# Performance work log

Measured on AMD Instinct MI355X. Metric: run time of the kernel, lower is better.

Reference implementation:

```python
import jax, jax.numpy as jnp
import numpy as np
import math

EMBED_DIM = 1024
NUM_HEADS = 16
HEAD_DIM = EMBED_DIM // NUM_HEADS
TGT_LEN = 1024
BSZ = 4


def setup_inputs() -> dict:
    key = jax.random.key(0)
    ks = jax.random.split(key, 7)
    # xavier_uniform for in_proj_weight [3E, E]
    limit = math.sqrt(6.0 / (3 * EMBED_DIM + EMBED_DIM))
    in_proj_weight = jax.random.uniform(ks[0], (3 * EMBED_DIM, EMBED_DIM), jnp.float32, -limit, limit)
    in_proj_bias = jnp.zeros((3 * EMBED_DIM,), jnp.float32)
    # out_proj: torch Linear default init (kaiming-uniform-ish); bias zeroed by _reset_parameters
    lim_o = 1.0 / math.sqrt(EMBED_DIM)
    out_proj_weight = jax.random.uniform(ks[1], (EMBED_DIM, EMBED_DIM), jnp.float32, -lim_o, lim_o)
    out_proj_bias = jnp.zeros((EMBED_DIM,), jnp.float32)
    query = jax.random.normal(ks[2], (TGT_LEN, BSZ, EMBED_DIM), jnp.float32)
    key_t = jax.random.normal(ks[3], (TGT_LEN, BSZ, EMBED_DIM), jnp.float32)
    value = jax.random.normal(ks[4], (TGT_LEN, BSZ, EMBED_DIM), jnp.float32)
    return {"query": query, "key": key_t, "value": value,
            "in_proj_weight": in_proj_weight, "in_proj_bias": in_proj_bias,
            "out_proj_weight": out_proj_weight, "out_proj_bias": out_proj_bias}


def reference(query, key, value, in_proj_weight, in_proj_bias, out_proj_weight, out_proj_bias):
    tgt_len, bsz, embed_dim = query.shape
    src_len = key.shape[0]
    w_q, w_k, w_v = jnp.split(in_proj_weight, 3, axis=0)
    b_q, b_k, b_v = jnp.split(in_proj_bias, 3, axis=0)
    q = query @ w_q.T + b_q  # [T, B, E]
    k = key @ w_k.T + b_k    # [S, B, E]
    v = value @ w_v.T + b_v  # [S, B, E]
    # [T, B*H, D] -> [B*H, T, D]
    q = q.reshape(tgt_len, bsz * NUM_HEADS, HEAD_DIM).transpose(1, 0, 2)
    k = k.reshape(src_len, bsz * NUM_HEADS, HEAD_DIM).transpose(1, 0, 2)
    v = v.reshape(src_len, bsz * NUM_HEADS, HEAD_DIM).transpose(1, 0, 2)
    q = q / math.sqrt(embed_dim)  # NOTE: scales by sqrt(embed_dim), not head_dim (faithful)
    attn = jax.nn.sigmoid(jnp.einsum('btd,bsd->bts', q, k))  # [B*H, T, S]
    attn_output = jnp.einsum('bts,bsd->btd', attn, v)         # [B*H, T, D]
    attn_output = attn_output.transpose(1, 0, 2).reshape(tgt_len, bsz, embed_dim)
    attn_output = attn_output @ out_proj_weight.T + out_proj_bias
    return attn_output, attn
```

## Files before the change

### kernel.cpp

```cpp
#include <hip/hip_runtime.h>
#include <stdint.h>

typedef unsigned short u16;
typedef __bf16 bf16x8 __attribute__((ext_vector_type(8)));
typedef float f32x4 __attribute__((ext_vector_type(4)));

__device__ __forceinline__ u16 f2bf(float f) {
  union { float f; uint32_t u; } v; v.f = f;
  uint32_t u = v.u;
  return (u16)((u + 0x7FFFu + ((u >> 16) & 1u)) >> 16);
}

__device__ __forceinline__ float fast_sigmoid(float x) {
  float e = __builtin_amdgcn_exp2f(x * -1.4426950408889634f);
  return __builtin_amdgcn_rcpf(1.0f + e);
}

__device__ __forceinline__ void cp16(const void* g, void* lds) {
  __builtin_amdgcn_global_load_lds(
      (const __attribute__((address_space(1))) uint32_t*)(uintptr_t)g,
      (__attribute__((address_space(3))) uint32_t*)(uint32_t)(uintptr_t)lds,
      16, 0, 0);
}

__global__ __launch_bounds__(256) void cvt_all(
    const float* __restrict__ q, const float* __restrict__ k,
    const float* __restrict__ v, const float* __restrict__ iw,
    const float* __restrict__ ow, u16* __restrict__ xq,
    u16* __restrict__ win, u16* __restrict__ wout) {
  int i = blockIdx.x * 256 + threadIdx.x;
  const float* s;
  u16* d;
  int off;
  if (i < 2097152) {
    if (i < 1048576) { s = q; d = xq; off = i; }
    else { s = k; d = xq + 4194304; off = i - 1048576; }
  } else if (i < 3145728) { s = v; d = xq + 8388608; off = i - 2097152; }
  else if (i < 3932160) { s = iw; d = win; off = i - 3145728; }
  else { s = ow; d = wout; off = i - 3932160; }
  float4 f = ((const float4*)s)[off];
  uint2 p;
  p.x = (uint32_t)f2bf(f.x) | ((uint32_t)f2bf(f.y) << 16);
  p.y = (uint32_t)f2bf(f.z) | ((uint32_t)f2bf(f.w) << 16);
  ((uint2*)d)[off] = p;
}

__device__ __forceinline__ void gemm128(const u16* __restrict__ A,
                                        const u16* __restrict__ Bt,
                                        int m0, int n0, int K,
                                        u16* As, u16* Bs, f32x4 acc[4][4]) {
  const int tid = threadIdx.x;
  const int l = tid & 63, w = tid >> 6;
  const int wr = w >> 1, wc = w & 1;
  const int quad = l >> 4, c = l & 15;
  const f32x4 zero = {0.f, 0.f, 0.f, 0.f};
  for (int i = 0; i < 4; ++i)
    for (int j = 0; j < 4; ++j) acc[i][j] = zero;

  for (int k0 = 0; k0 < K; k0 += 64) {
    __syncthreads();
#pragma unroll
    for (int p = 0; p < 4; ++p) {
      int q = p * 256 + tid;
      int row = q >> 3;
      int jj = (q & 7) ^ (row & 7);
      int ldsbase = (p * 256 + (tid & ~63)) * 8;
      cp16(A + (size_t)(m0 + row) * K + k0 + jj * 8, As + ldsbase);
      cp16(Bt + (size_t)(n0 + row) * K + k0 + jj * 8, Bs + ldsbase);
    }
    __syncthreads();
#pragma unroll
    for (int kk = 0; kk < 2; ++kk) {
      bf16x8 af[4], bf[4];
#pragma unroll
      for (int mt = 0; mt < 4; ++mt) {
        int row = wr * 64 + mt * 16 + c;
        af[mt] = *(const bf16x8*)(As + row * 64 + ((((kk << 2) + quad)) ^ (c & 7)) * 8);
      }
#pragma unroll
      for (int nt = 0; nt < 4; ++nt) {
        int row = wc * 64 + nt * 16 + c;
        bf[nt] = *(const bf16x8*)(Bs + row * 64 + ((((kk << 2) + quad)) ^ (c & 7)) * 8);
      }
#pragma unroll
      for (int mt = 0; mt < 4; ++mt)
#pragma unroll
        for (int nt = 0; nt < 4; ++nt)
          acc[mt][nt] = __builtin_amdgcn_mfma_f32_16x16x32_bf16(
              af[mt], bf[nt], acc[mt][nt], 0, 0, 0);
    }
  }
}

__global__ __launch_bounds__(256, 2) void proj_kernel(
    const u16* __restrict__ X, const u16* __restrict__ Win,
    const float* __restrict__ in_bias, u16* __restrict__ Q,
    u16* __restrict__ Kp, u16* __restrict__ Vtmp) {
  __shared__ u16 As[8192], Bs[8192];
  const int which = blockIdx.z;
  const u16* A = X + (size_t)which * (4096 * 1024);
  const u16* Bt = Win + (size_t)which * (1024 * 1024);
  const int m0 = blockIdx.y * 128, n0 = blockIdx.x * 128;
  f32x4 acc[4][4];
  gemm128(A, Bt, m0, n0, 1024, As, Bs, acc);

  u16* dst = (which == 0) ? Q : ((which == 1) ? Kp : Vtmp);
  const float scale = (which == 0) ? 0.03125f : 1.0f;
  const float* bias = in_bias + which * 1024;
  const int l = threadIdx.x & 63, w = threadIdx.x >> 6;
  const int wr = w >> 1, wc = w & 1, quad = l >> 4, c = l & 15;
#pragma unroll
  for (int mt = 0; mt < 4; ++mt)
#pragma unroll
    for (int nt = 0; nt < 4; ++nt) {
      int n = n0 + wc * 64 + nt * 16 + c;
      float bv = bias[n];
      int h = n >> 6, d = n & 63;
#pragma unroll
      for (int r = 0; r < 4; ++r) {
        int m = m0 + wr * 64 + mt * 16 + quad * 4 + r;
        int t = m >> 2, b = m & 3;
        dst[((size_t)((b * 16 + h) * 1024 + t)) * 64 + d] =
            f2bf((acc[mt][nt][r] + bv) * scale);
      }
    }
}

__global__ __launch_bounds__(256, 2) void outproj_kernel(
    const u16* __restrict__ AO, const u16* __restrict__ Wout,
    const float* __restrict__ out_bias, float* __restrict__ out) {
  __shared__ u16 As[8192], Bs[8192];
  const int m0 = blockIdx.y * 128, n0 = blockIdx.x * 128;
  f32x4 acc[4][4];
  gemm128(AO, Wout, m0, n0, 1024, As, Bs, acc);
  const int l = threadIdx.x & 63, w = threadIdx.x >> 6;
  const int wr = w >> 1, wc = w & 1, quad = l >> 4, c = l & 15;
#pragma unroll
  for (int mt = 0; mt < 4; ++mt)
#pragma unroll
    for (int nt = 0; nt < 4; ++nt) {
      int n = n0 + wc * 64 + nt * 16 + c;
      float bv = out_bias[n];
#pragma unroll
      for (int r = 0; r < 4; ++r) {
        int m = m0 + wr * 64 + mt * 16 + quad * 4 + r;
        __builtin_nontemporal_store(acc[mt][nt][r] + bv, &out[(size_t)m * 1024 + n]);
      }
    }
}

__global__ __launch_bounds__(256) void transpose_v(const u16* __restrict__ Vtmp,
                                                   u16* __restrict__ Vt) {
  __shared__ u16 tile[64 * 72];
  const int bh = blockIdx.y, s0 = blockIdx.x * 64;
  const u16* src = Vtmp + (size_t)bh * 65536;
  u16* dst = Vt + (size_t)bh * 65536;
#pragma unroll
  for (int p = 0; p < 2; ++p) {
    int q = p * 256 + threadIdx.x;
    int sl = q >> 3, dc = q & 7;
    uint4 v = *(const uint4*)(src + (size_t)(s0 + sl) * 64 + dc * 8);
    *(uint4*)&tile[sl * 72 + dc * 8] = v;
  }
  __syncthreads();
#pragma unroll
  for (int p = 0; p < 2; ++p) {
    int q = p * 256 + threadIdx.x;
    int d = q >> 3, sc = q & 7;
    u16 vals[8] __attribute__((aligned(16)));
#pragma unroll
    for (int j = 0; j < 8; ++j) vals[j] = tile[(sc * 8 + j) * 72 + d];
    *(uint4*)(dst + (size_t)d * 1024 + s0 + sc * 8) = *(const uint4*)vals;
  }
}

__global__ __launch_bounds__(256, 2) void attn_kernel(
    const u16* __restrict__ Q, const u16* __restrict__ Kg,
    const u16* __restrict__ Vt, float* __restrict__ attn_out,
    u16* __restrict__ AO) {
  extern __shared__ u16 smem[];
  u16* Qs = smem;
  u16* Ks = smem + 8192;
  u16* Vts = smem + 16384;
  u16* Ps = smem + 24576;
  const int bh = blockIdx.y, t0 = blockIdx.x * 128;
  const int b = bh >> 4, h = bh & 15;
  const int tid = threadIdx.x, l = tid & 63, w = tid >> 6;
  const int quad = l >> 4, c = l & 15;
  const int wr = w >> 1, wc = w & 1;
  const u16* Qbh = Q + (size_t)bh * 65536;
  const u16* Kbh = Kg + (size_t)bh * 65536;
  const u16* Vtbh = Vt + (size_t)bh * 65536;
  float* attnb = attn_out + (size_t)bh * 1048576;

#pragma unroll
  for (int p = 0; p < 4; ++p) {
    int q = p * 256 + tid;
    int row = q >> 3, jj = (q & 7) ^ (row & 7);
    cp16(Qbh + (size_t)(t0 + row) * 64 + jj * 8, Qs + (p * 256 + (tid & ~63)) * 8);
  }

  const f32x4 zero = {0.f, 0.f, 0.f, 0.f};
  f32x4 acc_o[2][4];
  for (int i = 0; i < 2; ++i)
    for (int j = 0; j < 4; ++j) acc_o[i][j] = zero;

  for (int s0 = 0; s0 < 1024; s0 += 128) {
    __syncthreads();
#pragma unroll
    for (int p = 0; p < 4; ++p) {
      int q = p * 256 + tid;
      int row = q >> 3, jj = (q & 7) ^ (row & 7);
      cp16(Kbh + (size_t)(s0 + row) * 64 + jj * 8, Ks + (p * 256 + (tid & ~63)) * 8);
    }
#pragma unroll
    for (int p = 0; p < 4; ++p) {
      int q = p * 256 + tid;
      int d = q >> 4, sc = q & 15;
      uint4 v = *(const uint4*)(Vtbh + (size_t)d * 1024 + s0 + sc * 8);
      *(uint4*)&Vts[d * 128 + (sc ^ (d & 15)) * 8] = v;
    }
    __syncthreads();

    f32x4 accp[4][4];
    for (int i = 0; i < 4; ++i)
      for (int j = 0; j < 4; ++j) accp[i][j] = zero;
#pragma unroll
    for (int kk = 0; kk < 2; ++kk) {
      bf16x8 af[4], bf[4];
#pragma unroll
      for (int mt = 0; mt < 4; ++mt) {
        int row = wr * 64 + mt * 16 + c;
        af[mt] = *(const bf16x8*)(Ks + row * 64 + (((kk << 2) + quad) ^ (c & 7)) * 8);
      }
#pragma unroll
      for (int nt = 0; nt < 4; ++nt) {
        int row = wc * 64 + nt * 16 + c;
        bf[nt] = *(const bf16x8*)(Qs + row * 64 + (((kk << 2) + quad) ^ (c & 7)) * 8);
      }
#pragma unroll
      for (int mt = 0; mt < 4; ++mt)
#pragma unroll
        for (int nt = 0; nt < 4; ++nt)
          accp[mt][nt] = __builtin_amdgcn_mfma_f32_16x16x32_bf16(
              af[mt], bf[nt], accp[mt][nt], 0, 0, 0);
    }

#pragma unroll
    for (int mt = 0; mt < 4; ++mt) {
      int sbase = wr * 64 + mt * 16 + quad * 4;
      int jw = sbase >> 3, hf = (sbase >> 2) & 1;
#pragma unroll
      for (int nt = 0; nt < 4; ++nt) {
        int t = wc * 64 + nt * 16 + c;
        f32x4 pv;
#pragma unroll
        for (int r = 0; r < 4; ++r) pv[r] = fast_sigmoid(accp[mt][nt][r]);
        accp[mt][nt] = pv;
        int jj = jw ^ (t & 15);
        uint2 pk;
        pk.x = (uint32_t)f2bf(pv[0]) | ((uint32_t)f2bf(pv[1]) << 16);
        pk.y = (uint32_t)f2bf(pv[2]) | ((uint32_t)f2bf(pv[3]) << 16);
        *(uint2*)&Ps[t * 128 + jj * 8 + hf * 4] = pk;
      }
    }
    __syncthreads();

#pragma unroll
    for (int mt = 0; mt < 4; ++mt) {
      int sl = wr * 64 + mt * 16 + quad * 4;
#pragma unroll
      for (int nt = 0; nt < 4; ++nt) {
        int t = wc * 64 + nt * 16 + c;
        __builtin_nontemporal_store(
            accp[mt][nt], (f32x4*)(attnb + (size_t)(t0 + t) * 1024 + s0 + sl));
      }
    }

#pragma unroll
    for (int kk = 0; kk < 4; ++kk) {
      bf16x8 ap[2], bv[4];
#pragma unroll
      for (int mt = 0; mt < 2; ++mt) {
        int row = w * 32 + mt * 16 + c;
        ap[mt] = *(const bf16x8*)(Ps + row * 128 + (((kk << 2) + quad) ^ (row & 15)) * 8);
      }
#pragma unroll
      for (int nt = 0; nt < 4; ++nt) {
        int d = nt * 16 + c;
        bv[nt] = *(const bf16x8*)(Vts + d * 128 + (((kk << 2) + quad) ^ (d & 15)) * 8);
      }
#pragma unroll
      for (int mt = 0; mt < 2; ++mt)
#pragma unroll
        for (int nt = 0; nt < 4; ++nt)
          acc_o[mt][nt] = __builtin_amdgcn_mfma_f32_16x16x32_bf16(
              ap[mt], bv[nt], acc_o[mt][nt], 0, 0, 0);
    }
  }

#pragma unroll
  for (int mt = 0; mt < 2; ++mt)
#pragma unroll
    for (int nt = 0; nt < 4; ++nt) {
      int d = nt * 16 + c;
#pragma unroll
      for (int r = 0; r < 4; ++r) {
        int t = t0 + w * 32 + mt * 16 + quad * 4 + r;
        AO[(size_t)(t * 4 + b) * 1024 + h * 64 + d] = f2bf(acc_o[mt][nt][r]);
      }
    }
}

extern "C" void kernel_launch(void* const* d_in, const int* in_sizes, int n_in,
                              void* d_out, int out_size, void* d_ws, size_t ws_size,
                              hipStream_t stream) {
  const float* query = (const float*)d_in[0];
  const float* key = (const float*)d_in[1];
  const float* value = (const float*)d_in[2];
  const float* in_w = (const float*)d_in[3];
  const float* in_b = (const float*)d_in[4];
  const float* out_w = (const float*)d_in[5];
  const float* out_b = (const float*)d_in[6];
  float* out = (float*)d_out;

  u16* ws = (u16*)d_ws;
  u16* xq = ws;
  u16* win = ws + 12582912;
  u16* wout = ws + 15728640;
  u16* Qp = ws + 16777216;
  u16* Kp = ws + 20971520;
  u16* Vt = ws + 25165824;
  u16* Vtmp = ws + 29360128;
  u16* AO = ws + 33554432;

  hipFuncSetAttribute((const void*)attn_kernel,
                      hipFuncAttributeMaxDynamicSharedMemorySize, 81920);

  cvt_all<<<16384, 256, 0, stream>>>(query, key, value, in_w, out_w, xq, win, wout);
  proj_kernel<<<dim3(8, 32, 3), 256, 0, stream>>>(xq, win, in_b, Qp, Kp, Vtmp);
  transpose_v<<<dim3(16, 64), 256, 0, stream>>>(Vtmp, Vt);
  attn_kernel<<<dim3(8, 64), 256, 81920, stream>>>(Qp, Kp, Vt, out + 4194304, AO);
  outproj_kernel<<<dim3(8, 32), 256, 0, stream>>>(AO, wout, out_b, out);
}
```

Measured before the change: 470.5 us.

## Fuse V transpose into projection epilogue and retile out-projection to 128x64

The V projection epilogue now writes its result directly in transposed [bh, d, t] layout, so the separate transpose_v kernel and the Vtmp buffer are gone. That saves one launch plus a full read and write of V. The out-projection GEMM is changed to 128x64 tiles with a 2x4 MFMA layout per wave, doubling the grid to 512 blocks for better CU occupancy on the small GEMM. The cost is that the transposed V stores are scattered 2-byte writes with poor coalescing, and the smaller tiles give less operand reuse.

```diff
diff --git a/kernel.cpp b/kernel.cpp
--- a/kernel.cpp
+++ b/kernel.cpp
@@ -95,7 +95,7 @@
 __global__ __launch_bounds__(256, 2) void proj_kernel(
     const u16* __restrict__ X, const u16* __restrict__ Win,
     const float* __restrict__ in_bias, u16* __restrict__ Q,
-    u16* __restrict__ Kp, u16* __restrict__ Vtmp) {
+    u16* __restrict__ Kp, u16* __restrict__ Vt) {
   __shared__ u16 As[8192], Bs[8192];
   const int which = blockIdx.z;
   const u16* A = X + (size_t)which * (4096 * 1024);
@@ -104,7 +104,6 @@
   f32x4 acc[4][4];
   gemm128(A, Bt, m0, n0, 1024, As, Bs, acc);
 
-  u16* dst = (which == 0) ? Q : ((which == 1) ? Kp : Vtmp);
   const float scale = (which == 0) ? 0.03125f : 1.0f;
   const float* bias = in_bias + which * 1024;
   const int l = threadIdx.x & 63, w = threadIdx.x >> 6;
@@ -120,8 +119,13 @@
       for (int r = 0; r < 4; ++r) {
         int m = m0 + wr * 64 + mt * 16 + quad * 4 + r;
         int t = m >> 2, b = m & 3;
-        dst[((size_t)((b * 16 + h) * 1024 + t)) * 64 + d] =
-            f2bf((acc[mt][nt][r] + bv) * scale);
+        u16 val = f2bf((acc[mt][nt][r] + bv) * scale);
+        if (which == 2) {
+          Vt[((size_t)(b * 16 + h) * 64 + d) * 1024 + t] = val;
+        } else {
+          u16* dst = (which == 0) ? Q : Kp;
+          dst[((size_t)((b * 16 + h) * 1024 + t)) * 64 + d] = val;
+        }
       }
     }
 }
@@ -129,49 +133,66 @@
 __global__ __launch_bounds__(256, 2) void outproj_kernel(
     const u16* __restrict__ AO, const u16* __restrict__ Wout,
     const float* __restrict__ out_bias, float* __restrict__ out) {
-  __shared__ u16 As[8192], Bs[8192];
-  const int m0 = blockIdx.y * 128, n0 = blockIdx.x * 128;
-  f32x4 acc[4][4];
-  gemm128(AO, Wout, m0, n0, 1024, As, Bs, acc);
-  const int l = threadIdx.x & 63, w = threadIdx.x >> 6;
-  const int wr = w >> 1, wc = w & 1, quad = l >> 4, c = l & 15;
-#pragma unroll
-  for (int mt = 0; mt < 4; ++mt)
+  __shared__ u16 As[8192];
+  __shared__ u16 Bs[4096];
+  const int m0 = blockIdx.y * 128, n0 = blockIdx.x * 64;
+  const int tid = threadIdx.x, l = tid & 63, w = tid >> 6;
+  const int quad = l >> 4, c = l & 15;
+  const f32x4 zero = {0.f, 0.f, 0.f, 0.f};
+  f32x4 acc[2][4];
+  for (int i = 0; i < 2; ++i)
+    for (int j = 0; j < 4; ++j) acc[i][j] = zero;
+
+  for (int k0 = 0; k0 < 1024; k0 += 64) {
+    __syncthreads();
+#pragma unroll
+    for (int p = 0; p < 4; ++p) {
+      int q = p * 256 + tid;
+      int row = q >> 3, jj = (q & 7) ^ (row & 7);
+      cp16(AO + (size_t)(m0 + row) * 1024 + k0 + jj * 8,
+           As + (p * 256 + (tid & ~63)) * 8);
+    }
+#pragma unroll
+    for (int p = 0; p < 2; ++p) {
+      int q = p * 256 + tid;
+      int row = q >> 3, jj = (q & 7) ^ (row & 7);
+      cp16(Wout + (size_t)(n0 + row) * 1024 + k0 + jj * 8,
+           Bs + (p * 256 + (tid & ~63)) * 8);
+    }
+    __syncthreads();
+#pragma unroll
+    for (int kk = 0; kk < 2; ++kk) {
+      bf16x8 af[2], bf[4];
+#pragma unroll
+      for (int mt = 0; mt < 2; ++mt) {
+        int row = w * 32 + mt * 16 + c;
+        af[mt] = *(const bf16x8*)(As + row * 64 + (((kk << 2) + quad) ^ (c & 7)) * 8);
+      }
+#pragma unroll
+      for (int nt = 0; nt < 4; ++nt) {
+        int row = nt * 16 + c;
+        bf[nt] = *(const bf16x8*)(Bs + row * 64 + (((kk << 2) + quad) ^ (c & 7)) * 8);
+      }
+#pragma unroll
+      for (int mt = 0; mt < 2; ++mt)
+#pragma unroll
+        for (int nt = 0; nt < 4; ++nt)
+          acc[mt][nt] = __builtin_amdgcn_mfma_f32_16x16x32_bf16(
+              af[mt], bf[nt], acc[mt][nt], 0, 0, 0);
+    }
+  }
+#pragma unroll
+  for (int mt = 0; mt < 2; ++mt)
 #pragma unroll
     for (int nt = 0; nt < 4; ++nt) {
-      int n = n0 + wc * 64 + nt * 16 + c;
+      int n = n0 + nt * 16 + c;
       float bv = out_bias[n];
 #pragma unroll
       for (int r = 0; r < 4; ++r) {
-        int m = m0 + wr * 64 + mt * 16 + quad * 4 + r;
+        int m = m0 + w * 32 + mt * 16 + quad * 4 + r;
         __builtin_nontemporal_store(acc[mt][nt][r] + bv, &out[(size_t)m * 1024 + n]);
       }
     }
-}
-
-__global__ __launch_bounds__(256) void transpose_v(const u16* __restrict__ Vtmp,
-                                                   u16* __restrict__ Vt) {
-  __shared__ u16 tile[64 * 72];
-  const int bh = blockIdx.y, s0 = blockIdx.x * 64;
-  const u16* src = Vtmp + (size_t)bh * 65536;
-  u16* dst = Vt + (size_t)bh * 65536;
-#pragma unroll
-  for (int p = 0; p < 2; ++p) {
-    int q = p * 256 + threadIdx.x;
-    int sl = q >> 3, dc = q & 7;
-    uint4 v = *(const uint4*)(src + (size_t)(s0 + sl) * 64 + dc * 8);
-    *(uint4*)&tile[sl * 72 + dc * 8] = v;
-  }
-  __syncthreads();
-#pragma unroll
-  for (int p = 0; p < 2; ++p) {
-    int q = p * 256 + threadIdx.x;
-    int d = q >> 3, sc = q & 7;
-    u16 vals[8] __attribute__((aligned(16)));
-#pragma unroll
-    for (int j = 0; j < 8; ++j) vals[j] = tile[(sc * 8 + j) * 72 + d];
-    *(uint4*)(dst + (size_t)d * 1024 + s0 + sc * 8) = *(const uint4*)vals;
-  }
 }
 
 __global__ __launch_bounds__(256, 2) void attn_kernel(
@@ -331,15 +352,13 @@
   u16* Qp = ws + 16777216;
   u16* Kp = ws + 20971520;
   u16* Vt = ws + 25165824;
-  u16* Vtmp = ws + 29360128;
   u16* AO = ws + 33554432;
 
   hipFuncSetAttribute((const void*)attn_kernel,
                       hipFuncAttributeMaxDynamicSharedMemorySize, 81920);
 
   cvt_all<<<16384, 256, 0, stream>>>(query, key, value, in_w, out_w, xq, win, wout);
-  proj_kernel<<<dim3(8, 32, 3), 256, 0, stream>>>(xq, win, in_b, Qp, Kp, Vtmp);
-  transpose_v<<<dim3(16, 64), 256, 0, stream>>>(Vtmp, Vt);
+  proj_kernel<<<dim3(8, 32, 3), 256, 0, stream>>>(xq, win, in_b, Qp, Kp, Vt);
   attn_kernel<<<dim3(8, 64), 256, 81920, stream>>>(Qp, Kp, Vt, out + 4194304, AO);
-  outproj_kernel<<<dim3(8, 32), 256, 0, stream>>>(AO, wout, out_b, out);
-}
+  outproj_kernel<<<dim3(16, 32), 256, 0, stream>>>(AO, wout, out_b, out);
+}
```

Result: no change. 462.1 us (-1.8%).
